# Optimization experiments

Measured on AMD Instinct MI355X. Metric: run time of the kernel, lower is better.

The kernel has to match this reference:

```python
import jax, jax.numpy as jnp
import numpy as np
from jax import lax

B, C_IN, T = 1024, 9, 2048
RT = T // 4            # reduced timesteps after two MaxPool(2)
HID, OUT = 128, 64
N_NODES = B * RT


def _chain_edges(rt, batch):
    """Bidirectional chain graph per sample, offset per batch element (PyG fallback)."""
    i = np.arange(rt - 1)
    src = np.concatenate([i, i + 1])   # edge_index[0] = source j
    dst = np.concatenate([i + 1, i])   # edge_index[1] = target i
    off = (np.arange(batch) * rt)[:, None]
    src = (src[None, :] + off).reshape(-1)
    dst = (dst[None, :] + off).reshape(-1)
    # degree with self-loops (GCNConv adds self-loops): endpoints 2, interior 3
    deg = np.full(rt, 3.0, np.float32)
    deg[0] = deg[-1] = 2.0
    deg = np.tile(deg, batch)
    return jnp.asarray(src, jnp.int32), jnp.asarray(dst, jnp.int32), jnp.asarray(deg ** -0.5)


def _conv1d(x, w, b):
    # x: [B, Cin, T], w: [Cout, Cin, 5] -> [B, Cout, T] (padding=2)
    y = lax.conv_general_dilated(x, w, window_strides=(1,), padding=[(2, 2)],
                                 dimension_numbers=('NCH', 'OIH', 'NCH'))
    return y + b[None, :, None]


def _maxpool2(x):
    b, c, t = x.shape
    return x.reshape(b, c, t // 2, 2).max(axis=-1)


def _gcn(x, W, b, src, dst, dinv):
    # GCNConv: x' = D^-1/2 (A+I) D^-1/2 (x W) + b
    h = x @ W                                        # [N, F]
    norm_e = (dinv[src] * dinv[dst])[:, None]        # per-edge sym norm
    agg = jax.ops.segment_sum(h[src] * norm_e, dst, num_segments=h.shape[0])
    return agg + h * (dinv * dinv)[:, None] + b      # self-loop term: 1/deg


def setup_inputs() -> dict:
    key = jax.random.key(0)
    ks = jax.random.split(key, 12)
    s = lambda k, shp, sc: jax.random.normal(k, shp, jnp.float32) * sc
    return {
        'x': jax.random.normal(ks[0], (B, C_IN, T), jnp.float32),
        'conv1_w': s(ks[1], (16, C_IN, 5), 0.15), 'conv1_b': jnp.zeros((16,), jnp.float32),
        'conv2_w': s(ks[2], (32, 16, 5), 0.1),   'conv2_b': jnp.zeros((32,), jnp.float32),
        'gcn1_w': s(ks[3], (32, HID), 0.17),     'gcn1_b': jnp.zeros((HID,), jnp.float32),
        'gcn2_w': s(ks[4], (HID, HID), 0.09),    'gcn2_b': jnp.zeros((HID,), jnp.float32),
        'fc_w': s(ks[5], (HID, OUT), 0.09),      'fc_b': jnp.zeros((OUT,), jnp.float32),
    }


def reference(x, conv1_w, conv1_b, conv2_w, conv2_b,
              gcn1_w, gcn1_b, gcn2_w, gcn2_b, fc_w, fc_b):
    b, c, t = x.shape
    h = _maxpool2(jax.nn.relu(_conv1d(x, conv1_w, conv1_b)))   # [B,16,T/2]
    h = _maxpool2(jax.nn.relu(_conv1d(h, conv2_w, conv2_b)))   # [B,32,T/4]
    rt = h.shape[-1]
    h = jnp.transpose(h, (0, 2, 1)).reshape(b * rt, 32)        # [N,32]
    src, dst, dinv = _chain_edges(rt, b)
    h = jax.nn.relu(_gcn(h, gcn1_w, gcn1_b, src, dst, dinv))
    h = jax.nn.relu(_gcn(h, gcn2_w, gcn2_b, src, dst, dinv))
    h = h.reshape(b, rt, -1).mean(axis=1)                      # [B,HID]
    return h @ fc_w + fc_b                                     # [B,OUT]
```

## Files before the change

### kernel.cpp

```cpp
#include <hip/hip_runtime.h>
#include <hip/hip_bf16.h>

#define B_      1024
#define CIN     9
#define T0_     2048
#define C1_     16
#define C2_     32
#define RT_     512
#define NNODES  (B_ * RT_)
#define HID_    128
#define OUTF_   64

typedef __attribute__((ext_vector_type(8))) __bf16 bf16x8;
typedef __attribute__((ext_vector_type(4))) float f32x4;
typedef __attribute__((ext_vector_type(8))) unsigned short us8;

__device__ __forceinline__ float bf2f(unsigned short u) {
    union { unsigned int i; float f; } c; c.i = ((unsigned int)u) << 16; return c.f;
}
__device__ __forceinline__ unsigned short f2bf1(float f) {
    union { float f; unsigned int i; } c; c.f = f;
    return (unsigned short)((c.i + 0x8000u) >> 16);
}
__device__ __forceinline__ unsigned int f2bf2(float lo, float hi) {
    union { float f; unsigned int i; } a, b; a.f = lo; b.f = hi;
    return __builtin_amdgcn_perm(b.i + 0x8000u, a.i + 0x8000u, 0x07060302u);
}
__device__ __forceinline__ float dinv_of(int r) {
    return (r == 0 || r == RT_ - 1) ? 0.70710678118f : 0.57735026919f;
}

__global__ __launch_bounds__(256) void repack_w(
    const float* __restrict__ W1g, const float* __restrict__ W2g,
    const float* __restrict__ Wc1g, const float* __restrict__ Wc2g,
    unsigned short* __restrict__ Wb1, unsigned short* __restrict__ Wb2,
    unsigned short* __restrict__ Wc1, unsigned short* __restrict__ Wc2)
{
    const int tid = threadIdx.x;
    const int bid = blockIdx.x;
    if (bid < 8) {
        for (int i = tid; i < 512; i += 256) {
            int s = bid * 512 + i;
            int k = s >> 7, f = s & 127;
            int lane = ((k >> 3) << 4) + (f & 15);
            int e = (((f >> 4) * 64) + lane) * 8 + (k & 7);
            Wb1[e] = f2bf1(W1g[s]);
        }
    } else if (bid < 24) {
        for (int i = tid; i < 1024; i += 256) {
            int s = (bid - 8) * 1024 + i;
            int k = s >> 7, f = s & 127;
            int ks = k >> 5, lane = (((k >> 3) & 3) << 4) + (f & 15);
            int e = ((ks * 8 + (f >> 4)) * 64 + lane) * 8 + (k & 7);
            Wb2[e] = f2bf1(W2g[s]);
        }
    } else if (bid < 28) {
        for (int i = tid; i < 384; i += 256) {
            int e = (bid - 24) * 384 + i;
            int j = e & 7, lane = (e >> 3) & 63, ks = e >> 9;
            int kk = ks * 32 + (lane >> 4) * 8 + j;
            int k = kk >> 4, ci = kk & 15, co = lane & 15;
            Wc1[e] = (k < 5 && ci < CIN) ? f2bf1(Wc1g[(co * CIN + ci) * 5 + k]) : 0;
        }
    } else {
        for (int i = tid; i < 768; i += 256) {
            int e = (bid - 28) * 768 + i;
            int j = e & 7, lane = (e >> 3) & 63, nt = (e >> 9) & 1, ks = e >> 10;
            int kk = ks * 32 + (lane >> 4) * 8 + j;
            int k = kk >> 4, ci = kk & 15, co = nt * 16 + (lane & 15);
            Wc2[e] = (k < 5) ? f2bf1(Wc2g[(co * C1_ + ci) * 5 + k]) : 0;
        }
    }
}

__global__ __launch_bounds__(256, 3) void mega(
    const float* __restrict__ x,
    const unsigned short* __restrict__ Wc1,
    const unsigned short* __restrict__ Wc2,
    const unsigned short* __restrict__ Wb1,
    const unsigned short* __restrict__ Wb2,
    const float* __restrict__ c1b, const float* __restrict__ c2b,
    const float* __restrict__ g1b, const float* __restrict__ g2b,
    float* __restrict__ partials)
{
    __shared__ __align__(16) unsigned char lds[49856];
    unsigned short* xs    = (unsigned short*)(lds);
    unsigned short* y2loc = (unsigned short*)(lds);
    unsigned short* H     = (unsigned short*)(lds);
    unsigned short* y1ext = (unsigned short*)(lds + 35392);
    unsigned short* As1   = (unsigned short*)(lds + 35392);
    unsigned short* A2q   = (unsigned short*)(lds + 35392);
    float* bls1 = (float*)(lds + 48832);
    float* bls2 = (float*)(lds + 49344);

    const int tid = threadIdx.x;
    const int b = blockIdx.x >> 2;
    const int r0 = (blockIdx.x & 3) * 128;
    if (tid < 128) { bls1[tid] = g1b[tid]; bls2[tid] = g2b[tid]; }

    const int lane = tid & 63, wave = tid >> 6;
    const int m = lane & 15, q = lane >> 4;

    bf16x8 wfB[3];
    #pragma unroll
    for (int ks = 0; ks < 3; ks++) wfB[ks] = *(const bf16x8*)(Wc1 + (ks * 64 + lane) * 8);
    bf16x8 wfC[3][2];
    #pragma unroll
    for (int ks = 0; ks < 3; ks++)
        #pragma unroll
        for (int nt = 0; nt < 2; nt++)
            wfC[ks][nt] = *(const bf16x8*)(Wc2 + ((ks * 2 + nt) * 64 + lane) * 8);

    {
        const float* xb = x + (size_t)b * CIN * T0_;
        const int xbase = 4 * r0 - 14;
        for (int s = tid; s < 552; s += 256) {
            const int xt = xbase + s;
            union { us8 v; unsigned int u[4]; } o0, o1;
            if (xt >= 0 && xt < T0_) {
                float xv[9];
                #pragma unroll
                for (int ci = 0; ci < 9; ci++) xv[ci] = xb[ci * T0_ + xt];
                o0.u[0] = f2bf2(xv[0], xv[1]); o0.u[1] = f2bf2(xv[2], xv[3]);
                o0.u[2] = f2bf2(xv[4], xv[5]); o0.u[3] = f2bf2(xv[6], xv[7]);
                o1.u[0] = f2bf2(xv[8], 0.f);   o1.u[1] = o1.u[2] = o1.u[3] = 0;
            } else {
                o0.u[0] = o0.u[1] = o0.u[2] = o0.u[3] = 0;
                o1.u[0] = o1.u[1] = o1.u[2] = o1.u[3] = 0;
            }
            *(us8*)(xs + s * 24) = o0.v;
            *(us8*)(xs + s * 24 + 8) = o1.v;
        }
    }
    __syncthreads();

    {
        const float bv = c1b[m];
        const int t1base = 2 * r0 - 6;
        for (int mt = wave; mt < 34; mt += 4) {
            f32x4 acc = {};
            #pragma unroll
            for (int ks = 0; ks < 3; ks++) {
                const int row = mt * 16 + m + ks * 2 + (q >> 1);
                const bf16x8 af = *(const bf16x8*)(xs + row * 24 + (q & 1) * 8);
                acc = __builtin_amdgcn_mfma_f32_16x16x32_bf16(af, wfB[ks], acc, 0, 0, 0);
            }
            const int prow = mt * 8 + q * 2;
            const int t1a = t1base + prow, t1b = t1a + 1;
            const float p0 = fmaxf(fmaxf(acc[0], acc[1]) + bv, 0.f);
            const float p1 = fmaxf(fmaxf(acc[2], acc[3]) + bv, 0.f);
            if (prow < 268)
                y1ext[prow * 24 + m] = (t1a >= 0 && t1a < 1024) ? f2bf1(p0) : (unsigned short)0;
            if (prow + 1 < 268)
                y1ext[(prow + 1) * 24 + m] = (t1b >= 0 && t1b < 1024) ? f2bf1(p1) : (unsigned short)0;
        }
        for (int idx = tid; idx < 288; idx += 256) y1ext[268 * 24 + idx] = 0;
    }
    __syncthreads();

    {
        const float bv0 = c2b[m], bv1 = c2b[16 + m];
        for (int mt = wave; mt < 17; mt += 4) {
            f32x4 a0 = {}, a1 = {};
            #pragma unroll
            for (int ks = 0; ks < 3; ks++) {
                const int row = mt * 16 + m + ks * 2 + (q >> 1);
                const bf16x8 af = *(const bf16x8*)(y1ext + row * 24 + (q & 1) * 8);
                a0 = __builtin_amdgcn_mfma_f32_16x16x32_bf16(af, wfC[ks][0], a0, 0, 0, 0);
                a1 = __builtin_amdgcn_mfma_f32_16x16x32_bf16(af, wfC[ks][1], a1, 0, 0, 0);
            }
            const int nrow = mt * 8 + q * 2;
            if (nrow < 132) {
                y2loc[nrow * 40 + m]      = f2bf1(fmaxf(fmaxf(a0[0], a0[1]) + bv0, 0.f));
                y2loc[nrow * 40 + 16 + m] = f2bf1(fmaxf(fmaxf(a1[0], a1[1]) + bv1, 0.f));
            }
            if (nrow + 1 < 132) {
                y2loc[(nrow + 1) * 40 + m]      = f2bf1(fmaxf(fmaxf(a0[2], a0[3]) + bv0, 0.f));
                y2loc[(nrow + 1) * 40 + 16 + m] = f2bf1(fmaxf(fmaxf(a1[2], a1[3]) + bv1, 0.f));
            }
        }
    }
    bf16x8 wfE[2];
    {
        const int ft0 = wave * 2;
        wfE[0] = *(const bf16x8*)(Wb1 + (ft0 * 64 + lane) * 8);
        wfE[1] = *(const bf16x8*)(Wb1 + ((ft0 + 1) * 64 + lane) * 8);
    }
    __syncthreads();

    for (int s = tid; s < 288; s += 256) {
        const int i = s >> 1, fh = (s & 1) * 16;
        unsigned short* dst = As1 + i * 40 + fh;
        const int r = r0 - 1 + i;
        union { us8 v; unsigned int u[4]; } o0, o1;
        if (i >= 130 || r < 0 || r >= RT_) {
            o0.u[0] = o0.u[1] = o0.u[2] = o0.u[3] = 0;
            o1.u[0] = o1.u[1] = o1.u[2] = o1.u[3] = 0;
        } else {
            const float dm = dinv_of(r), cm = dm * dm;
            const unsigned short* Yc = y2loc + (i + 1) * 40 + fh;
            us8 c0 = *(const us8*)(Yc), c1 = *(const us8*)(Yc + 8);
            float v[16];
            #pragma unroll
            for (int j = 0; j < 8; j++) { v[j] = cm * bf2f(c0[j]); v[8 + j] = cm * bf2f(c1[j]); }
            if (r > 0) {
                const float cl = dm * dinv_of(r - 1);
                us8 a0 = *(const us8*)(Yc - 40), a1 = *(const us8*)(Yc - 32);
                #pragma unroll
                for (int j = 0; j < 8; j++) { v[j] += cl * bf2f(a0[j]); v[8 + j] += cl * bf2f(a1[j]); }
            }
            if (r < RT_ - 1) {
                const float cr = dm * dinv_of(r + 1);
                us8 a0 = *(const us8*)(Yc + 40), a1 = *(const us8*)(Yc + 48);
                #pragma unroll
                for (int j = 0; j < 8; j++) { v[j] += cr * bf2f(a0[j]); v[8 + j] += cr * bf2f(a1[j]); }
            }
            #pragma unroll
            for (int i2 = 0; i2 < 4; i2++) {
                o0.u[i2] = f2bf2(v[2 * i2], v[2 * i2 + 1]);
                o1.u[i2] = f2bf2(v[8 + 2 * i2], v[9 + 2 * i2]);
            }
        }
        *(us8*)dst = o0.v; *(us8*)(dst + 8) = o1.v;
    }
    bf16x8 bw[4][2];
    #pragma unroll
    for (int ks = 0; ks < 4; ks++)
        #pragma unroll
        for (int i = 0; i < 2; i++)
            bw[ks][i] = *(const bf16x8*)(Wb2 + ((size_t)((ks * 8 + wave * 2 + i) * 64 + lane)) * 8);
    __syncthreads();

    {
        const int ft0 = wave * 2;
        const float4 bv0 = *(const float4*)&bls1[ft0 * 16 + q * 4];
        const float4 bv1 = *(const float4*)&bls1[(ft0 + 1) * 16 + q * 4];
        #pragma unroll
        for (int nt = 0; nt < 9; nt++) {
            const bf16x8 bfr = *(const bf16x8*)(As1 + (nt * 16 + m) * 40 + q * 8);
            f32x4 a0 = {}, a1 = {};
            a0 = __builtin_amdgcn_mfma_f32_16x16x32_bf16(wfE[0], bfr, a0, 0, 0, 0);
            a1 = __builtin_amdgcn_mfma_f32_16x16x32_bf16(wfE[1], bfr, a1, 0, 0, 0);
            const int row = nt * 16 + m;
            if (row < 130) {
                union { ushort4 s; unsigned int u[2]; } o0, o1;
                o0.u[0] = f2bf2(fmaxf(a0[0] + bv0.x, 0.f), fmaxf(a0[1] + bv0.y, 0.f));
                o0.u[1] = f2bf2(fmaxf(a0[2] + bv0.z, 0.f), fmaxf(a0[3] + bv0.w, 0.f));
                o1.u[0] = f2bf2(fmaxf(a1[0] + bv1.x, 0.f), fmaxf(a1[1] + bv1.y, 0.f));
                o1.u[1] = f2bf2(fmaxf(a1[2] + bv1.z, 0.f), fmaxf(a1[3] + bv1.w, 0.f));
                *(ushort4*)(H + row * 136 + ft0 * 16 + q * 4) = o0.s;
                *(ushort4*)(H + row * 136 + (ft0 + 1) * 16 + q * 4) = o1.s;
            }
        }
    }
    __syncthreads();

    f32x4 acc[8][2] = {};
    #pragma unroll
    for (int qi = 0; qi < 4; qi++) {
        {
            const int jl = tid >> 3, fh = (tid & 7) * 16;
            const int j = qi * 32 + jl;
            const int r = r0 + j;
            const float dm = dinv_of(r), cm = dm * dm;
            const float cl = (r > 0) ? dm * dinv_of(r - 1) : 0.f;
            const float cr = (r < RT_ - 1) ? dm * dinv_of(r + 1) : 0.f;
            const unsigned short* Hl = H + j * 136 + fh;
            const unsigned short* Hc = Hl + 136;
            const unsigned short* Hr = Hc + 136;
            unsigned short* dst = A2q + jl * 152 + fh;
            #pragma unroll
            for (int c = 0; c < 2; c++) {
                us8 cc = *(const us8*)(Hc + c * 8);
                us8 ll = *(const us8*)(Hl + c * 8);
                us8 rr = *(const us8*)(Hr + c * 8);
                float v[8];
                #pragma unroll
                for (int e = 0; e < 8; e++)
                    v[e] = cm * bf2f(cc[e]) + cl * bf2f(ll[e]) + cr * bf2f(rr[e]);
                union { us8 v; unsigned int u[4]; } o;
                #pragma unroll
                for (int i2 = 0; i2 < 4; i2++) o.u[i2] = f2bf2(v[2 * i2], v[2 * i2 + 1]);
                *(us8*)(dst + c * 8) = o.v;
            }
        }
        __syncthreads();
        #pragma unroll
        for (int ntl = 0; ntl < 2; ntl++) {
            const int nt = qi * 2 + ntl;
            #pragma unroll
            for (int ks = 0; ks < 4; ks++) {
                const bf16x8 af = *(const bf16x8*)(A2q + (ntl * 16 + m) * 152 + ks * 32 + q * 8);
                acc[nt][0] = __builtin_amdgcn_mfma_f32_16x16x32_bf16(af, bw[ks][0], acc[nt][0], 0, 0, 0);
                acc[nt][1] = __builtin_amdgcn_mfma_f32_16x16x32_bf16(af, bw[ks][1], acc[nt][1], 0, 0, 0);
            }
        }
        if (qi < 3) __syncthreads();
    }

    {
        const float bb0 = bls2[wave * 32 + m];
        const float bb1 = bls2[wave * 32 + 16 + m];
        float s0 = 0.f, s1 = 0.f;
        #pragma unroll
        for (int nt = 0; nt < 8; nt++)
            #pragma unroll
            for (int rgi = 0; rgi < 4; rgi++) {
                s0 += fmaxf(acc[nt][0][rgi] + bb0, 0.f);
                s1 += fmaxf(acc[nt][1][rgi] + bb1, 0.f);
            }
        s0 += __shfl_xor(s0, 16, 64); s0 += __shfl_xor(s0, 32, 64);
        s1 += __shfl_xor(s1, 16, 64); s1 += __shfl_xor(s1, 32, 64);
        if (lane < 16) {
            float* p = partials + (size_t)blockIdx.x * 128 + wave * 32;
            p[m] = s0;
            p[16 + m] = s1;
        }
    }
}

__global__ __launch_bounds__(128) void fc_kernel(
    const float* __restrict__ partials, const float* __restrict__ fw,
    const float* __restrict__ fb, float* __restrict__ out)
{
    __shared__ float sm[128];
    const int b = blockIdx.x, tid = threadIdx.x;
    float s = 0.f;
    #pragma unroll
    for (int t = 0; t < 4; t++) s += partials[((b << 2) + t) * 128 + tid];
    sm[tid] = s * (1.0f / 512.0f);
    __syncthreads();
    if (tid < 64) {
        float acc = fb[tid];
        #pragma unroll 8
        for (int f = 0; f < 128; f++) acc += sm[f] * fw[f * 64 + tid];
        out[b * 64 + tid] = acc;
    }
}

extern "C" void kernel_launch(void* const* d_in, const int* in_sizes, int n_in,
                              void* d_out, int out_size, void* d_ws, size_t ws_size,
                              hipStream_t stream)
{
    const float* x   = (const float*)d_in[0];
    const float* w1  = (const float*)d_in[1];
    const float* b1  = (const float*)d_in[2];
    const float* w2  = (const float*)d_in[3];
    const float* b2  = (const float*)d_in[4];
    const float* g1w = (const float*)d_in[5];
    const float* g1b = (const float*)d_in[6];
    const float* g2w = (const float*)d_in[7];
    const float* g2b = (const float*)d_in[8];
    const float* fw  = (const float*)d_in[9];
    const float* fb  = (const float*)d_in[10];

    char* ws = (char*)d_ws;
    float* partials     = (float*)(ws);
    unsigned short* Wb1 = (unsigned short*)(ws + 2097152);
    unsigned short* Wb2 = (unsigned short*)(ws + 2097152 + 16384);
    unsigned short* Wc1 = (unsigned short*)(ws + 2097152 + 65536);
    unsigned short* Wc2 = (unsigned short*)(ws + 2097152 + 81920);
    float* out = (float*)d_out;

    repack_w<<<32, 256, 0, stream>>>(g1w, g2w, w1, w2, Wb1, Wb2, Wc1, Wc2);
    mega<<<NNODES / 128, 256, 0, stream>>>(x, Wc1, Wc2, Wb1, Wb2,
                                           b1, b2, g1b, g2b, partials);
    fc_kernel<<<B_, 128, 0, stream>>>(partials, fw, fb, out);
}
```

Baseline: 191.2 us.

## Compute GCN neighbor aggregation with banded MFMA and stream GCN2 over feature chunks

```diff
diff --git a/kernel.cpp b/kernel.cpp
--- a/kernel.cpp
+++ b/kernel.cpp
@@ -28,6 +28,27 @@
 }
 __device__ __forceinline__ float dinv_of(int r) {
     return (r == 0 || r == RT_ - 1) ? 0.70710678118f : 0.57735026919f;
+}
+
+__device__ __forceinline__ void band3(int rbase, int n, int g, bf16x8* hi, bf16x8* lo) {
+    const int r = rbase + n;
+    float cl = 0.f, cm = 0.f, cr = 0.f;
+    if (r >= 0 && r < RT_) {
+        const float dm = dinv_of(r);
+        cl = (r > 0)        ? 3.f * dm * dinv_of(r - 1) : 0.f;
+        cm = 3.f * dm * dm;
+        cr = (r < RT_ - 1)  ? 3.f * dm * dinv_of(r + 1) : 0.f;
+    }
+    union { us8 u; bf16x8 b; } h, l;
+    #pragma unroll
+    for (int j = 0; j < 8; j++) {
+        const int d = (g * 8 + j) - n;
+        const float c = (d == 0) ? cl : (d == 1) ? cm : (d == 2) ? cr : 0.f;
+        const unsigned short ch = f2bf1(c);
+        h.u[j] = ch;
+        l.u[j] = f2bf1(c - bf2f(ch));
+    }
+    *hi = h.b; *lo = l.b;
 }
 
 __global__ __launch_bounds__(256) void repack_w(
@@ -73,7 +94,7 @@
     }
 }
 
-__global__ __launch_bounds__(256, 3) void mega(
+__global__ __launch_bounds__(256, 4) void mega(
     const float* __restrict__ x,
     const unsigned short* __restrict__ Wc1,
     const unsigned short* __restrict__ Wc2,
@@ -83,33 +104,27 @@
     const float* __restrict__ g1b, const float* __restrict__ g2b,
     float* __restrict__ partials)
 {
-    __shared__ __align__(16) unsigned char lds[49856];
+    __shared__ __align__(16) unsigned char lds[38912];
     unsigned short* xs    = (unsigned short*)(lds);
-    unsigned short* y2loc = (unsigned short*)(lds);
-    unsigned short* H     = (unsigned short*)(lds);
-    unsigned short* y1ext = (unsigned short*)(lds + 35392);
-    unsigned short* As1   = (unsigned short*)(lds + 35392);
-    unsigned short* A2q   = (unsigned short*)(lds + 35392);
-    float* bls1 = (float*)(lds + 48832);
-    float* bls2 = (float*)(lds + 49344);
+    unsigned short* y1ext = (unsigned short*)(lds + 26496);
+    unsigned short* y2T   = (unsigned short*)(lds);
+    unsigned short* As1   = (unsigned short*)(lds + 10752);
+    unsigned short* HTs   = (unsigned short*)(lds + 19968);
+    unsigned short* A2s   = (unsigned short*)(lds + 29696);
+    float* bls1 = (float*)(lds + 37888);
+    float* bls2 = (float*)(lds + 38400);
 
     const int tid = threadIdx.x;
     const int b = blockIdx.x >> 2;
     const int r0 = (blockIdx.x & 3) * 128;
-    if (tid < 128) { bls1[tid] = g1b[tid]; bls2[tid] = g2b[tid]; }
 
     const int lane = tid & 63, wave = tid >> 6;
     const int m = lane & 15, q = lane >> 4;
+    const int wp = wave & 1;
 
     bf16x8 wfB[3];
     #pragma unroll
     for (int ks = 0; ks < 3; ks++) wfB[ks] = *(const bf16x8*)(Wc1 + (ks * 64 + lane) * 8);
-    bf16x8 wfC[3][2];
-    #pragma unroll
-    for (int ks = 0; ks < 3; ks++)
-        #pragma unroll
-        for (int nt = 0; nt < 2; nt++)
-            wfC[ks][nt] = *(const bf16x8*)(Wc2 + ((ks * 2 + nt) * 64 + lane) * 8);
 
     {
         const float* xb = x + (size_t)b * CIN * T0_;
@@ -132,6 +147,12 @@
             *(us8*)(xs + s * 24 + 8) = o1.v;
         }
     }
+    bf16x8 wfC[3][2];
+    #pragma unroll
+    for (int ks = 0; ks < 3; ks++)
+        #pragma unroll
+        for (int nt = 0; nt < 2; nt++)
+            wfC[ks][nt] = *(const bf16x8*)(Wc2 + ((ks * 2 + nt) * 64 + lane) * 8);
     __syncthreads();
 
     {
@@ -159,6 +180,10 @@
     __syncthreads();
 
     {
+        for (int i = tid; i < 512; i += 256) {
+            const int row = i >> 4, c = i & 15;
+            *(unsigned int*)(y2T + row * 168 + 132 + c * 2) = 0u;
+        }
         const float bv0 = c2b[m], bv1 = c2b[16 + m];
         for (int mt = wave; mt < 17; mt += 4) {
             f32x4 a0 = {}, a1 = {};
@@ -171,131 +196,95 @@
             }
             const int nrow = mt * 8 + q * 2;
             if (nrow < 132) {
-                y2loc[nrow * 40 + m]      = f2bf1(fmaxf(fmaxf(a0[0], a0[1]) + bv0, 0.f));
-                y2loc[nrow * 40 + 16 + m] = f2bf1(fmaxf(fmaxf(a1[0], a1[1]) + bv1, 0.f));
+                y2T[m * 168 + nrow]        = f2bf1(fmaxf(fmaxf(a0[0], a0[1]) + bv0, 0.f));
+                y2T[(16 + m) * 168 + nrow] = f2bf1(fmaxf(fmaxf(a1[0], a1[1]) + bv1, 0.f));
             }
             if (nrow + 1 < 132) {
-                y2loc[(nrow + 1) * 40 + m]      = f2bf1(fmaxf(fmaxf(a0[2], a0[3]) + bv0, 0.f));
-                y2loc[(nrow + 1) * 40 + 16 + m] = f2bf1(fmaxf(fmaxf(a1[2], a1[3]) + bv1, 0.f));
-            }
-        }
-    }
-    bf16x8 wfE[2];
-    {
-        const int ft0 = wave * 2;
-        wfE[0] = *(const bf16x8*)(Wb1 + (ft0 * 64 + lane) * 8);
-        wfE[1] = *(const bf16x8*)(Wb1 + ((ft0 + 1) * 64 + lane) * 8);
-    }
-    __syncthreads();
-
-    for (int s = tid; s < 288; s += 256) {
-        const int i = s >> 1, fh = (s & 1) * 16;
-        unsigned short* dst = As1 + i * 40 + fh;
-        const int r = r0 - 1 + i;
-        union { us8 v; unsigned int u[4]; } o0, o1;
-        if (i >= 130 || r < 0 || r >= RT_) {
-            o0.u[0] = o0.u[1] = o0.u[2] = o0.u[3] = 0;
-            o1.u[0] = o1.u[1] = o1.u[2] = o1.u[3] = 0;
+                y2T[m * 168 + nrow + 1]        = f2bf1(fmaxf(fmaxf(a0[2], a0[3]) + bv0, 0.f));
+                y2T[(16 + m) * 168 + nrow + 1] = f2bf1(fmaxf(fmaxf(a1[2], a1[3]) + bv1, 0.f));
+            }
+        }
+    }
+    __syncthreads();
+
+    union { us8 u; bf16x8 b; } bones;
+    #pragma unroll
+    for (int j = 0; j < 8; j++) {
+        const int d = (q * 8 + j) - m;
+        bones.u[j] = (d >= 0 && d <= 2) ? (unsigned short)0x3F80 : (unsigned short)0;
+    }
+    const f32x4 zz = {};
+
+    if (tid < 128) { bls1[tid] = g1b[tid]; bls2[tid] = g2b[tid]; }
+    for (int idx = wave; idx < 18; idx += 4) {
+        const int ot = idx >> 1;
+        const bf16x8 af = *(const bf16x8*)(y2T + (wp * 16 + m) * 168 + ot * 16 + q * 8);
+        f32x4 o;
+        if ((r0 == 0 && ot == 0) || (r0 == 384 && ot >= 7)) {
+            bf16x8 bh, bl; band3(r0 - 1 + ot * 16, m, q, &bh, &bl);
+            o = __builtin_amdgcn_mfma_f32_16x16x32_bf16(af, bh, zz, 0, 0, 0);
+            o = __builtin_amdgcn_mfma_f32_16x16x32_bf16(af, bl, o, 0, 0, 0);
         } else {
-            const float dm = dinv_of(r), cm = dm * dm;
-            const unsigned short* Yc = y2loc + (i + 1) * 40 + fh;
-            us8 c0 = *(const us8*)(Yc), c1 = *(const us8*)(Yc + 8);
-            float v[16];
-            #pragma unroll
-            for (int j = 0; j < 8; j++) { v[j] = cm * bf2f(c0[j]); v[8 + j] = cm * bf2f(c1[j]); }
-            if (r > 0) {
-                const float cl = dm * dinv_of(r - 1);
-                us8 a0 = *(const us8*)(Yc - 40), a1 = *(const us8*)(Yc - 32);
-                #pragma unroll
-                for (int j = 0; j < 8; j++) { v[j] += cl * bf2f(a0[j]); v[8 + j] += cl * bf2f(a1[j]); }
-            }
-            if (r < RT_ - 1) {
-                const float cr = dm * dinv_of(r + 1);
-                us8 a0 = *(const us8*)(Yc + 40), a1 = *(const us8*)(Yc + 48);
-                #pragma unroll
-                for (int j = 0; j < 8; j++) { v[j] += cr * bf2f(a0[j]); v[8 + j] += cr * bf2f(a1[j]); }
-            }
-            #pragma unroll
-            for (int i2 = 0; i2 < 4; i2++) {
-                o0.u[i2] = f2bf2(v[2 * i2], v[2 * i2 + 1]);
-                o1.u[i2] = f2bf2(v[8 + 2 * i2], v[9 + 2 * i2]);
-            }
-        }
-        *(us8*)dst = o0.v; *(us8*)(dst + 8) = o1.v;
-    }
-    bf16x8 bw[4][2];
-    #pragma unroll
-    for (int ks = 0; ks < 4; ks++)
+            o = __builtin_amdgcn_mfma_f32_16x16x32_bf16(af, bones.b, zz, 0, 0, 0);
+        }
+        union { ushort4 s; unsigned int u[2]; } w;
+        w.u[0] = f2bf2(o[0] * (1.f / 3.f), o[1] * (1.f / 3.f));
+        w.u[1] = f2bf2(o[2] * (1.f / 3.f), o[3] * (1.f / 3.f));
+        *(ushort4*)(As1 + (ot * 16 + m) * 32 + wp * 16 + q * 4) = w.s;
+    }
+    __syncthreads();
+
+    f32x4 acc[8][2] = {};
+    bf16x8 wfE = *(const bf16x8*)(Wb1 + ((size_t)(wp * 64 + lane)) * 8);
+    bf16x8 bwA = *(const bf16x8*)(Wb2 + ((size_t)((wave * 2 + 0) * 64 + lane)) * 8);
+    bf16x8 bwB = *(const bf16x8*)(Wb2 + ((size_t)((wave * 2 + 1) * 64 + lane)) * 8);
+
+    for (int ks = 0; ks < 4; ks++) {
+        {
+            const float4 bv = *(const float4*)&bls1[ks * 32 + wp * 16 + q * 4];
+            for (int idx = wave; idx < 18; idx += 4) {
+                const int nt = idx >> 1;
+                const bf16x8 bfr = *(const bf16x8*)(As1 + (nt * 16 + m) * 32 + q * 8);
+                f32x4 o = __builtin_amdgcn_mfma_f32_16x16x32_bf16(wfE, bfr, zz, 0, 0, 0);
+                unsigned short* hb = HTs + (wp * 16 + q * 4) * 152 + nt * 16 + m;
+                hb[0]   = f2bf1(fmaxf(o[0] + bv.x, 0.f));
+                hb[152] = f2bf1(fmaxf(o[1] + bv.y, 0.f));
+                hb[304] = f2bf1(fmaxf(o[2] + bv.z, 0.f));
+                hb[456] = f2bf1(fmaxf(o[3] + bv.w, 0.f));
+            }
+        }
+        const int ksn = (ks < 3) ? ks + 1 : 3;
+        bf16x8 nE = *(const bf16x8*)(Wb1 + ((size_t)((2 * ksn + wp) * 64 + lane)) * 8);
+        bf16x8 nA = *(const bf16x8*)(Wb2 + ((size_t)((ksn * 8 + wave * 2 + 0) * 64 + lane)) * 8);
+        bf16x8 nB = *(const bf16x8*)(Wb2 + ((size_t)((ksn * 8 + wave * 2 + 1) * 64 + lane)) * 8);
+        __syncthreads();
+
+        for (int idx = wave; idx < 16; idx += 4) {
+            const int nt = idx >> 1;
+            const bf16x8 af = *(const bf16x8*)(HTs + (wp * 16 + m) * 152 + nt * 16 + q * 8);
+            f32x4 o;
+            if ((r0 == 0 && nt == 0) || (r0 == 384 && nt == 7)) {
+                bf16x8 bh, bl; band3(r0 + nt * 16, m, q, &bh, &bl);
+                o = __builtin_amdgcn_mfma_f32_16x16x32_bf16(af, bh, zz, 0, 0, 0);
+                o = __builtin_amdgcn_mfma_f32_16x16x32_bf16(af, bl, o, 0, 0, 0);
+            } else {
+                o = __builtin_amdgcn_mfma_f32_16x16x32_bf16(af, bones.b, zz, 0, 0, 0);
+            }
+            union { ushort4 s; unsigned int u[2]; } w;
+            w.u[0] = f2bf2(o[0] * (1.f / 3.f), o[1] * (1.f / 3.f));
+            w.u[1] = f2bf2(o[2] * (1.f / 3.f), o[3] * (1.f / 3.f));
+            *(ushort4*)(A2s + (nt * 16 + m) * 32 + wp * 16 + q * 4) = w.s;
+        }
+        __syncthreads();
+
         #pragma unroll
-        for (int i = 0; i < 2; i++)
-            bw[ks][i] = *(const bf16x8*)(Wb2 + ((size_t)((ks * 8 + wave * 2 + i) * 64 + lane)) * 8);
-    __syncthreads();
-
-    {
-        const int ft0 = wave * 2;
-        const float4 bv0 = *(const float4*)&bls1[ft0 * 16 + q * 4];
-        const float4 bv1 = *(const float4*)&bls1[(ft0 + 1) * 16 + q * 4];
-        #pragma unroll
-        for (int nt = 0; nt < 9; nt++) {
-            const bf16x8 bfr = *(const bf16x8*)(As1 + (nt * 16 + m) * 40 + q * 8);
-            f32x4 a0 = {}, a1 = {};
-            a0 = __builtin_amdgcn_mfma_f32_16x16x32_bf16(wfE[0], bfr, a0, 0, 0, 0);
-            a1 = __builtin_amdgcn_mfma_f32_16x16x32_bf16(wfE[1], bfr, a1, 0, 0, 0);
-            const int row = nt * 16 + m;
-            if (row < 130) {
-                union { ushort4 s; unsigned int u[2]; } o0, o1;
-                o0.u[0] = f2bf2(fmaxf(a0[0] + bv0.x, 0.f), fmaxf(a0[1] + bv0.y, 0.f));
-                o0.u[1] = f2bf2(fmaxf(a0[2] + bv0.z, 0.f), fmaxf(a0[3] + bv0.w, 0.f));
-                o1.u[0] = f2bf2(fmaxf(a1[0] + bv1.x, 0.f), fmaxf(a1[1] + bv1.y, 0.f));
-                o1.u[1] = f2bf2(fmaxf(a1[2] + bv1.z, 0.f), fmaxf(a1[3] + bv1.w, 0.f));
-                *(ushort4*)(H + row * 136 + ft0 * 16 + q * 4) = o0.s;
-                *(ushort4*)(H + row * 136 + (ft0 + 1) * 16 + q * 4) = o1.s;
-            }
-        }
-    }
-    __syncthreads();
-
-    f32x4 acc[8][2] = {};
-    #pragma unroll
-    for (int qi = 0; qi < 4; qi++) {
-        {
-            const int jl = tid >> 3, fh = (tid & 7) * 16;
-            const int j = qi * 32 + jl;
-            const int r = r0 + j;
-            const float dm = dinv_of(r), cm = dm * dm;
-            const float cl = (r > 0) ? dm * dinv_of(r - 1) : 0.f;
-            const float cr = (r < RT_ - 1) ? dm * dinv_of(r + 1) : 0.f;
-            const unsigned short* Hl = H + j * 136 + fh;
-            const unsigned short* Hc = Hl + 136;
-            const unsigned short* Hr = Hc + 136;
-            unsigned short* dst = A2q + jl * 152 + fh;
-            #pragma unroll
-            for (int c = 0; c < 2; c++) {
-                us8 cc = *(const us8*)(Hc + c * 8);
-                us8 ll = *(const us8*)(Hl + c * 8);
-                us8 rr = *(const us8*)(Hr + c * 8);
-                float v[8];
-                #pragma unroll
-                for (int e = 0; e < 8; e++)
-                    v[e] = cm * bf2f(cc[e]) + cl * bf2f(ll[e]) + cr * bf2f(rr[e]);
-                union { us8 v; unsigned int u[4]; } o;
-                #pragma unroll
-                for (int i2 = 0; i2 < 4; i2++) o.u[i2] = f2bf2(v[2 * i2], v[2 * i2 + 1]);
-                *(us8*)(dst + c * 8) = o.v;
-            }
-        }
+        for (int nt = 0; nt < 8; nt++) {
+            const bf16x8 af = *(const bf16x8*)(A2s + (nt * 16 + m) * 32 + q * 8);
+            acc[nt][0] = __builtin_amdgcn_mfma_f32_16x16x32_bf16(af, bwA, acc[nt][0], 0, 0, 0);
+            acc[nt][1] = __builtin_amdgcn_mfma_f32_16x16x32_bf16(af, bwB, acc[nt][1], 0, 0, 0);
+        }
+        wfE = nE; bwA = nA; bwB = nB;
         __syncthreads();
-        #pragma unroll
-        for (int ntl = 0; ntl < 2; ntl++) {
-            const int nt = qi * 2 + ntl;
-            #pragma unroll
-            for (int ks = 0; ks < 4; ks++) {
-                const bf16x8 af = *(const bf16x8*)(A2q + (ntl * 16 + m) * 152 + ks * 32 + q * 8);
-                acc[nt][0] = __builtin_amdgcn_mfma_f32_16x16x32_bf16(af, bw[ks][0], acc[nt][0], 0, 0, 0);
-                acc[nt][1] = __builtin_amdgcn_mfma_f32_16x16x32_bf16(af, bw[ks][1], acc[nt][1], 0, 0, 0);
-            }
-        }
-        if (qi < 3) __syncthreads();
     }
 
     {
```

Result: slower. 202.6 us (+5.9%).

## Stream GCN1 output per quarter to shrink LDS and raise occupancy

Applied to the files above, without the earlier changes.

```diff
diff --git a/kernel.cpp b/kernel.cpp
--- a/kernel.cpp
+++ b/kernel.cpp
@@ -73,7 +73,7 @@
     }
 }
 
-__global__ __launch_bounds__(256, 3) void mega(
+__global__ __launch_bounds__(256, 4) void mega(
     const float* __restrict__ x,
     const unsigned short* __restrict__ Wc1,
     const unsigned short* __restrict__ Wc2,
@@ -83,33 +83,25 @@
     const float* __restrict__ g1b, const float* __restrict__ g2b,
     float* __restrict__ partials)
 {
-    __shared__ __align__(16) unsigned char lds[49856];
+    __shared__ __align__(16) unsigned char lds[40032];
     unsigned short* xs    = (unsigned short*)(lds);
+    unsigned short* y1ext = (unsigned short*)(lds + 26496);
     unsigned short* y2loc = (unsigned short*)(lds);
-    unsigned short* H     = (unsigned short*)(lds);
-    unsigned short* y1ext = (unsigned short*)(lds + 35392);
-    unsigned short* As1   = (unsigned short*)(lds + 35392);
-    unsigned short* A2q   = (unsigned short*)(lds + 35392);
-    float* bls1 = (float*)(lds + 48832);
-    float* bls2 = (float*)(lds + 49344);
+    unsigned short* As1   = (unsigned short*)(lds + 10560);
+    unsigned short* Hq    = (unsigned short*)(lds + 22080);
+    unsigned short* A2q   = (unsigned short*)(lds + 31328);
 
     const int tid = threadIdx.x;
     const int b = blockIdx.x >> 2;
     const int r0 = (blockIdx.x & 3) * 128;
-    if (tid < 128) { bls1[tid] = g1b[tid]; bls2[tid] = g2b[tid]; }
 
     const int lane = tid & 63, wave = tid >> 6;
     const int m = lane & 15, q = lane >> 4;
+    const int ft0 = wave * 2;
 
     bf16x8 wfB[3];
     #pragma unroll
     for (int ks = 0; ks < 3; ks++) wfB[ks] = *(const bf16x8*)(Wc1 + (ks * 64 + lane) * 8);
-    bf16x8 wfC[3][2];
-    #pragma unroll
-    for (int ks = 0; ks < 3; ks++)
-        #pragma unroll
-        for (int nt = 0; nt < 2; nt++)
-            wfC[ks][nt] = *(const bf16x8*)(Wc2 + ((ks * 2 + nt) * 64 + lane) * 8);
 
     {
         const float* xb = x + (size_t)b * CIN * T0_;
@@ -132,6 +124,12 @@
             *(us8*)(xs + s * 24 + 8) = o1.v;
         }
     }
+    bf16x8 wfC[3][2];
+    #pragma unroll
+    for (int ks = 0; ks < 3; ks++)
+        #pragma unroll
+        for (int nt = 0; nt < 2; nt++)
+            wfC[ks][nt] = *(const bf16x8*)(Wc2 + ((ks * 2 + nt) * 64 + lane) * 8);
     __syncthreads();
 
     {
@@ -181,11 +179,8 @@
         }
     }
     bf16x8 wfE[2];
-    {
-        const int ft0 = wave * 2;
-        wfE[0] = *(const bf16x8*)(Wb1 + (ft0 * 64 + lane) * 8);
-        wfE[1] = *(const bf16x8*)(Wb1 + ((ft0 + 1) * 64 + lane) * 8);
-    }
+    wfE[0] = *(const bf16x8*)(Wb1 + (ft0 * 64 + lane) * 8);
+    wfE[1] = *(const bf16x8*)(Wb1 + ((ft0 + 1) * 64 + lane) * 8);
     __syncthreads();
 
     for (int s = tid; s < 288; s += 256) {
@@ -229,46 +224,48 @@
         #pragma unroll
         for (int i = 0; i < 2; i++)
             bw[ks][i] = *(const bf16x8*)(Wb2 + ((size_t)((ks * 8 + wave * 2 + i) * 64 + lane)) * 8);
-    __syncthreads();
-
-    {
-        const int ft0 = wave * 2;
-        const float4 bv0 = *(const float4*)&bls1[ft0 * 16 + q * 4];
-        const float4 bv1 = *(const float4*)&bls1[(ft0 + 1) * 16 + q * 4];
+    const float4 bv0 = *(const float4*)&g1b[ft0 * 16 + q * 4];
+    const float4 bv1 = *(const float4*)&g1b[(ft0 + 1) * 16 + q * 4];
+    const float bb0 = g2b[wave * 32 + m];
+    const float bb1 = g2b[wave * 32 + 16 + m];
+    __syncthreads();
+
+    const f32x4 zz = {};
+
+    auto do_E = [&](int qi) {
         #pragma unroll
-        for (int nt = 0; nt < 9; nt++) {
-            const bf16x8 bfr = *(const bf16x8*)(As1 + (nt * 16 + m) * 40 + q * 8);
-            f32x4 a0 = {}, a1 = {};
-            a0 = __builtin_amdgcn_mfma_f32_16x16x32_bf16(wfE[0], bfr, a0, 0, 0, 0);
-            a1 = __builtin_amdgcn_mfma_f32_16x16x32_bf16(wfE[1], bfr, a1, 0, 0, 0);
-            const int row = nt * 16 + m;
-            if (row < 130) {
-                union { ushort4 s; unsigned int u[2]; } o0, o1;
-                o0.u[0] = f2bf2(fmaxf(a0[0] + bv0.x, 0.f), fmaxf(a0[1] + bv0.y, 0.f));
-                o0.u[1] = f2bf2(fmaxf(a0[2] + bv0.z, 0.f), fmaxf(a0[3] + bv0.w, 0.f));
-                o1.u[0] = f2bf2(fmaxf(a1[0] + bv1.x, 0.f), fmaxf(a1[1] + bv1.y, 0.f));
-                o1.u[1] = f2bf2(fmaxf(a1[2] + bv1.z, 0.f), fmaxf(a1[3] + bv1.w, 0.f));
-                *(ushort4*)(H + row * 136 + ft0 * 16 + q * 4) = o0.s;
-                *(ushort4*)(H + row * 136 + (ft0 + 1) * 16 + q * 4) = o1.s;
-            }
-        }
-    }
-    __syncthreads();
-
-    f32x4 acc[8][2] = {};
-    #pragma unroll
+        for (int nt = 0; nt < 3; nt++) {
+            const bf16x8 bfr = *(const bf16x8*)(As1 + (qi * 32 + nt * 16 + m) * 40 + q * 8);
+            f32x4 o0 = __builtin_amdgcn_mfma_f32_16x16x32_bf16(wfE[0], bfr, zz, 0, 0, 0);
+            f32x4 o1 = __builtin_amdgcn_mfma_f32_16x16x32_bf16(wfE[1], bfr, zz, 0, 0, 0);
+            const int hrow = nt * 16 + m;
+            if (hrow < 34) {
+                union { ushort4 s; unsigned int u[2]; } w0, w1;
+                w0.u[0] = f2bf2(fmaxf(o0[0] + bv0.x, 0.f), fmaxf(o0[1] + bv0.y, 0.f));
+                w0.u[1] = f2bf2(fmaxf(o0[2] + bv0.z, 0.f), fmaxf(o0[3] + bv0.w, 0.f));
+                w1.u[0] = f2bf2(fmaxf(o1[0] + bv1.x, 0.f), fmaxf(o1[1] + bv1.y, 0.f));
+                w1.u[1] = f2bf2(fmaxf(o1[2] + bv1.z, 0.f), fmaxf(o1[3] + bv1.w, 0.f));
+                *(ushort4*)(Hq + hrow * 136 + ft0 * 16 + q * 4) = w0.s;
+                *(ushort4*)(Hq + hrow * 136 + (ft0 + 1) * 16 + q * 4) = w1.s;
+            }
+        }
+    };
+
+    do_E(0);
+    __syncthreads();
+
+    float s0 = 0.f, s1 = 0.f;
     for (int qi = 0; qi < 4; qi++) {
         {
             const int jl = tid >> 3, fh = (tid & 7) * 16;
-            const int j = qi * 32 + jl;
-            const int r = r0 + j;
+            const int r = r0 + qi * 32 + jl;
             const float dm = dinv_of(r), cm = dm * dm;
             const float cl = (r > 0) ? dm * dinv_of(r - 1) : 0.f;
             const float cr = (r < RT_ - 1) ? dm * dinv_of(r + 1) : 0.f;
-            const unsigned short* Hl = H + j * 136 + fh;
+            const unsigned short* Hl = Hq + jl * 136 + fh;
             const unsigned short* Hc = Hl + 136;
             const unsigned short* Hr = Hc + 136;
-            unsigned short* dst = A2q + jl * 152 + fh;
+            unsigned short* dst = A2q + jl * 136 + fh;
             #pragma unroll
             for (int c = 0; c < 2; c++) {
                 us8 cc = *(const us8*)(Hc + c * 8);
@@ -285,30 +282,32 @@
             }
         }
         __syncthreads();
-        #pragma unroll
-        for (int ntl = 0; ntl < 2; ntl++) {
-            const int nt = qi * 2 + ntl;
-            #pragma unroll
-            for (int ks = 0; ks < 4; ks++) {
-                const bf16x8 af = *(const bf16x8*)(A2q + (ntl * 16 + m) * 152 + ks * 32 + q * 8);
-                acc[nt][0] = __builtin_amdgcn_mfma_f32_16x16x32_bf16(af, bw[ks][0], acc[nt][0], 0, 0, 0);
-                acc[nt][1] = __builtin_amdgcn_mfma_f32_16x16x32_bf16(af, bw[ks][1], acc[nt][1], 0, 0, 0);
-            }
-        }
-        if (qi < 3) __syncthreads();
+
+        {
+            f32x4 acc2[2][2] = {};
+            #pragma unroll
+            for (int ntl = 0; ntl < 2; ntl++)
+                #pragma unroll
+                for (int ks = 0; ks < 4; ks++) {
+                    const bf16x8 af = *(const bf16x8*)(A2q + (ntl * 16 + m) * 136 + ks * 32 + q * 8);
+                    acc2[ntl][0] = __builtin_amdgcn_mfma_f32_16x16x32_bf16(af, bw[ks][0], acc2[ntl][0], 0, 0, 0);
+                    acc2[ntl][1] = __builtin_amdgcn_mfma_f32_16x16x32_bf16(af, bw[ks][1], acc2[ntl][1], 0, 0, 0);
+                }
+            #pragma unroll
+            for (int ntl = 0; ntl < 2; ntl++)
+                #pragma unroll
+                for (int rgi = 0; rgi < 4; rgi++) {
+                    s0 += fmaxf(acc2[ntl][0][rgi] + bb0, 0.f);
+                    s1 += fmaxf(acc2[ntl][1][rgi] + bb1, 0.f);
+                }
+        }
+        if (qi < 3) {
+            do_E(qi + 1);
+            __syncthreads();
+        }
     }
 
     {
-        const float bb0 = bls2[wave * 32 + m];
-        const float bb1 = bls2[wave * 32 + 16 + m];
-        float s0 = 0.f, s1 = 0.f;
-        #pragma unroll
-        for (int nt = 0; nt < 8; nt++)
-            #pragma unroll
-            for (int rgi = 0; rgi < 4; rgi++) {
-                s0 += fmaxf(acc[nt][0][rgi] + bb0, 0.f);
-                s1 += fmaxf(acc[nt][1][rgi] + bb1, 0.f);
-            }
         s0 += __shfl_xor(s0, 16, 64); s0 += __shfl_xor(s0, 32, 64);
         s1 += __shfl_xor(s1, 16, 64); s1 += __shfl_xor(s1, 32, 64);
         if (lane < 16) {
```

New measurement: 183.5 us, median of 2. 1.04x faster.
